# Kernel tuning notes

Hardware: AMD Instinct MI355X
Metric: run time of the kernel (lower is better)

The kernel has to match this reference:

```python
import jax, jax.numpy as jnp
import numpy as np

BN_EPS = 1e-5

def setup_inputs() -> dict:
    key = jax.random.key(0)
    k1, k2, k3 = jax.random.split(key, 3)
    N, T, C = 20000, 35, 4
    cin, cout = 7, 128
    h = cout // 2  # 64
    voxels = jax.random.normal(k1, (N, T, C), dtype=jnp.float32)
    # Linear params (torch default init scale ~ 1/sqrt(cin))
    W = jax.random.normal(k2, (h, cin), dtype=jnp.float32) / np.sqrt(cin)
    b = jax.random.normal(k3, (h,), dtype=jnp.float32) * 0.01
    gamma = jnp.ones((h,), dtype=jnp.float32)
    beta = jnp.zeros((h,), dtype=jnp.float32)
    return {"voxels": voxels, "W": W, "b": b, "gamma": gamma, "beta": beta}

def reference(voxels, W, b, gamma, beta):
    N, T, C = voxels.shape
    # mask of non-empty points: rows whose channel-sum is nonzero
    mask = (voxels.sum(axis=-1, keepdims=True) != 0)              # [N,T,1]
    counts = mask.sum(axis=1, keepdims=True).astype(voxels.dtype)  # [N,1,1]
    voxels_mean = voxels.sum(axis=1, keepdims=True) / counts       # [N,1,C]
    rel = voxels[:, :, :3] - voxels_mean[:, :, :3]                 # [N,T,3]
    aug = jnp.concatenate([voxels, rel], axis=-1)                  # [N,T,C+3]
    x = aug.reshape(-1, aug.shape[-1])                             # [N*T, 7]
    # Linear
    x = x @ W.T + b                                                # [N*T, h]
    # BatchNorm1d (training mode: batch stats, biased variance)
    mu = x.mean(axis=0)
    var = jnp.mean(jnp.square(x - mu), axis=0)
    x = (x - mu) / jnp.sqrt(var + BN_EPS) * gamma + beta
    # ReLU
    x = jnp.maximum(x, 0.0)
    x = x.reshape(N, T, -1)                                        # [N,T,h]
    agg = x.max(axis=1, keepdims=True)                             # [N,1,h]
    out = jnp.concatenate([x, jnp.broadcast_to(agg, x.shape)], axis=-1)  # [N,T,2h]
    return out
```

## Files before the change

kernel.cpp:

```cpp
#include <hip/hip_runtime.h>


#define NVOX   20000
#define TDIM   35
#define NCH    128
#define HID    64
#define NTF    700000.0f
#define EPS    1e-5f
#define NBLK_A 256
#define SCALE_OFF (NBLK_A * 35)
#define SHIFT_OFF (NBLK_A * 35 + 64)

__global__ __launch_bounds__(256) void vfe_stats(const float* __restrict__ vox,
                                                 float* __restrict__ ws) {
  const int lane = threadIdx.x & 63;
  const int wid  = threadIdx.x >> 6;
  const int gwave  = (blockIdx.x * 256 + threadIdx.x) >> 6;
  const int nwaves = NBLK_A * 4;

  float m2[28], sv[7];
#pragma unroll
  for (int i = 0; i < 28; ++i) m2[i] = 0.f;
#pragma unroll
  for (int i = 0; i < 7; ++i) sv[i] = 0.f;

  for (int n = gwave; n < NVOX; n += nwaves) {
    float4 row = make_float4(0.f, 0.f, 0.f, 0.f);
    if (lane < TDIM) row = *(const float4*)(vox + (size_t)n * (TDIM * 4) + lane * 4);
    float rowsum = (row.x + row.y) + (row.z + row.w);
    float cnt = (float)__popcll(__ballot((lane < TDIM) && (rowsum != 0.f)));
    float s0 = row.x, s1 = row.y, s2 = row.z;
#pragma unroll
    for (int off = 32; off; off >>= 1) {
      s0 += __shfl_down(s0, off);
      s1 += __shfl_down(s1, off);
      s2 += __shfl_down(s2, off);
    }
    float mx = __shfl(s0, 0) / cnt;
    float my = __shfl(s1, 0) / cnt;
    float mz = __shfl(s2, 0) / cnt;
    if (lane < TDIM) {
      float a[7] = {row.x, row.y, row.z, row.w, row.x - mx, row.y - my, row.z - mz};
      int idx = 0;
#pragma unroll
      for (int j = 0; j < 7; ++j) {
        sv[j] += a[j];
#pragma unroll
        for (int k = j; k < 7; ++k) { m2[idx] = fmaf(a[j], a[k], m2[idx]); ++idx; }
      }
    }
  }

  __shared__ float part[4][35];
#pragma unroll
  for (int i = 0; i < 35; ++i) {
    float v = (i < 28) ? m2[i] : sv[i - 28];
#pragma unroll
    for (int off = 32; off; off >>= 1) v += __shfl_down(v, off);
    if (lane == 0) part[wid][i] = v;
  }
  __syncthreads();
  if (threadIdx.x < 35)
    ws[blockIdx.x * 35 + threadIdx.x] =
        part[0][threadIdx.x] + part[1][threadIdx.x] +
        part[2][threadIdx.x] + part[3][threadIdx.x];
}

__global__ void vfe_bnparams(const float* __restrict__ W, const float* __restrict__ b,
                             const float* __restrict__ gamma, const float* __restrict__ beta,
                             float* __restrict__ ws) {
  __shared__ float stats[35];
  for (int i = threadIdx.x; i < 35; i += 64) {
    float acc = 0.f;
    for (int p = 0; p < NBLK_A; ++p) acc += ws[p * 35 + i];
    stats[i] = acc;
  }
  __syncthreads();

  const int c = threadIdx.x;
  float m2[7][7];
  {
    int idx = 0;
    for (int j = 0; j < 7; ++j)
      for (int k = j; k < 7; ++k) { float v = stats[idx++]; m2[j][k] = v; m2[k][j] = v; }
  }
  float w[7];
#pragma unroll
  for (int j = 0; j < 7; ++j) w[j] = W[c * 7 + j];
  float bc = b[c];

  float wdots = 0.f;
#pragma unroll
  for (int j = 0; j < 7; ++j) wdots = fmaf(w[j], stats[28 + j], wdots);
  float q = 0.f;
#pragma unroll
  for (int j = 0; j < 7; ++j) {
    float t = 0.f;
#pragma unroll
    for (int k = 0; k < 7; ++k) t = fmaf(w[k], m2[j][k], t);
    q = fmaf(w[j], t, q);
  }
  float sx  = wdots + NTF * bc;
  float sxx = q + 2.f * bc * wdots + NTF * bc * bc;
  float mu  = sx / NTF;
  float var = sxx / NTF - mu * mu;
  float scale = gamma[c] / sqrtf(var + EPS);
  float shift = beta[c] + scale * (bc - mu);
  ws[SCALE_OFF + c] = scale;
  ws[SHIFT_OFF + c] = shift;
}

__global__ __launch_bounds__(256) void vfe_encode(const float* __restrict__ vox,
                                                  const float* __restrict__ W,
                                                  const float* __restrict__ ws,
                                                  float* __restrict__ out) {
  const int lane = threadIdx.x & 63;
  const int n = (blockIdx.x * 256 + threadIdx.x) >> 6;
  if (n >= NVOX) return;

  float4 row = make_float4(0.f, 0.f, 0.f, 0.f);
  if (lane < TDIM) row = *(const float4*)(vox + (size_t)n * (TDIM * 4) + lane * 4);
  float rowsum = (row.x + row.y) + (row.z + row.w);
  float cnt = (float)__popcll(__ballot((lane < TDIM) && (rowsum != 0.f)));
  float s0 = row.x, s1 = row.y, s2 = row.z;
#pragma unroll
  for (int off = 32; off; off >>= 1) {
    s0 += __shfl_down(s0, off);
    s1 += __shfl_down(s1, off);
    s2 += __shfl_down(s2, off);
  }
  const float r4 = row.x - __shfl(s0, 0) / cnt;
  const float r5 = row.y - __shfl(s1, 0) / cnt;
  const float r6 = row.z - __shfl(s2, 0) / cnt;

  const float w0 = W[lane * 7 + 0], w1 = W[lane * 7 + 1], w2 = W[lane * 7 + 2],
              w3 = W[lane * 7 + 3], w4 = W[lane * 7 + 4], w5 = W[lane * 7 + 5],
              w6 = W[lane * 7 + 6];
  const float scale = ws[SCALE_OFF + lane];
  const float shift = ws[SHIFT_OFF + lane];

  float* op = out + (size_t)n * (TDIM * NCH) + lane;
  float agg = 0.f;
#pragma unroll
  for (int t = 0; t < TDIM; ++t) {
    float d = w0 * __shfl(row.x, t);
    d = fmaf(w1, __shfl(row.y, t), d);
    d = fmaf(w2, __shfl(row.z, t), d);
    d = fmaf(w3, __shfl(row.w, t), d);
    d = fmaf(w4, __shfl(r4, t), d);
    d = fmaf(w5, __shfl(r5, t), d);
    d = fmaf(w6, __shfl(r6, t), d);
    float y = fmaf(d, scale, shift);
    y = fmaxf(y, 0.f);
    agg = fmaxf(agg, y);
    op[t * NCH] = y;
  }
#pragma unroll
  for (int t = 0; t < TDIM; ++t) op[t * NCH + HID] = agg;
}

extern "C" void kernel_launch(void* const* d_in, const int* in_sizes, int n_in,
                              void* d_out, int out_size, void* d_ws, size_t ws_size,
                              hipStream_t stream) {
  const float* vox   = (const float*)d_in[0];
  const float* W     = (const float*)d_in[1];
  const float* b     = (const float*)d_in[2];
  const float* gamma = (const float*)d_in[3];
  const float* beta  = (const float*)d_in[4];
  float* out = (float*)d_out;
  float* ws  = (float*)d_ws;

  vfe_stats<<<NBLK_A, 256, 0, stream>>>(vox, ws);
  vfe_bnparams<<<1, 64, 0, stream>>>(W, b, gamma, beta, ws);
  vfe_encode<<<(NVOX * 64) / 256, 256, 0, stream>>>(vox, W, ws, out);
}
```

Baseline: 397.8 us.

## Fold BN scale into weights and vectorize encode stores via LDS-staged rows

The BN parameter kernel now folds scale into the linear weights and merges the relative-coordinate terms algebraically, so the encoder needs four FMAs per output plus a per-voxel base. The encode kernel stages each voxel's rows in shared memory and remaps lanes so each thread handles four channels across a quarter of the time steps. Output is written with float4 stores, which should give wider, coalesced writes on this output-bandwidth-bound kernel. It adds a block barrier and a cross-lane max reduction, and it relies on NVOX being divisible by 4 now that the bounds check is removed.

```diff
diff --git a/kernel.cpp b/kernel.cpp
--- a/kernel.cpp
+++ b/kernel.cpp
@@ -8,8 +8,7 @@
 #define NTF    700000.0f
 #define EPS    1e-5f
 #define NBLK_A 256
-#define SCALE_OFF (NBLK_A * 35)
-#define SHIFT_OFF (NBLK_A * 35 + 64)
+#define PARAM_OFF (NBLK_A * 35)
 
 __global__ __launch_bounds__(256) void vfe_stats(const float* __restrict__ vox,
                                                  float* __restrict__ ws) {
@@ -36,9 +35,10 @@
       s1 += __shfl_down(s1, off);
       s2 += __shfl_down(s2, off);
     }
-    float mx = __shfl(s0, 0) / cnt;
-    float my = __shfl(s1, 0) / cnt;
-    float mz = __shfl(s2, 0) / cnt;
+    float rc = 1.f / cnt;
+    float mx = __shfl(s0, 0) * rc;
+    float my = __shfl(s1, 0) * rc;
+    float mz = __shfl(s2, 0) * rc;
     if (lane < TDIM) {
       float a[7] = {row.x, row.y, row.z, row.w, row.x - mx, row.y - my, row.z - mz};
       int idx = 0;
@@ -106,17 +106,26 @@
   float var = sxx / NTF - mu * mu;
   float scale = gamma[c] / sqrtf(var + EPS);
   float shift = beta[c] + scale * (bc - mu);
-  ws[SCALE_OFF + c] = scale;
-  ws[SHIFT_OFF + c] = shift;
+
+  float* p = ws + PARAM_OFF + c * 8;
+  p[0] = scale * (w[0] + w[4]);
+  p[1] = scale * (w[1] + w[5]);
+  p[2] = scale * (w[2] + w[6]);
+  p[3] = scale * w[3];
+  p[4] = scale * w[4];
+  p[5] = scale * w[5];
+  p[6] = scale * w[6];
+  p[7] = shift;
 }
 
 __global__ __launch_bounds__(256) void vfe_encode(const float* __restrict__ vox,
-                                                  const float* __restrict__ W,
                                                   const float* __restrict__ ws,
                                                   float* __restrict__ out) {
   const int lane = threadIdx.x & 63;
+  const int wid  = threadIdx.x >> 6;
   const int n = (blockIdx.x * 256 + threadIdx.x) >> 6;
-  if (n >= NVOX) return;
+
+  __shared__ float4 rows[4][64];
 
   float4 row = make_float4(0.f, 0.f, 0.f, 0.f);
   if (lane < TDIM) row = *(const float4*)(vox + (size_t)n * (TDIM * 4) + lane * 4);
@@ -129,34 +138,60 @@
     s1 += __shfl_down(s1, off);
     s2 += __shfl_down(s2, off);
   }
-  const float r4 = row.x - __shfl(s0, 0) / cnt;
-  const float r5 = row.y - __shfl(s1, 0) / cnt;
-  const float r6 = row.z - __shfl(s2, 0) / cnt;
-
-  const float w0 = W[lane * 7 + 0], w1 = W[lane * 7 + 1], w2 = W[lane * 7 + 2],
-              w3 = W[lane * 7 + 3], w4 = W[lane * 7 + 4], w5 = W[lane * 7 + 5],
-              w6 = W[lane * 7 + 6];
-  const float scale = ws[SCALE_OFF + lane];
-  const float shift = ws[SHIFT_OFF + lane];
-
-  float* op = out + (size_t)n * (TDIM * NCH) + lane;
-  float agg = 0.f;
-#pragma unroll
-  for (int t = 0; t < TDIM; ++t) {
-    float d = w0 * __shfl(row.x, t);
-    d = fmaf(w1, __shfl(row.y, t), d);
-    d = fmaf(w2, __shfl(row.z, t), d);
-    d = fmaf(w3, __shfl(row.w, t), d);
-    d = fmaf(w4, __shfl(r4, t), d);
-    d = fmaf(w5, __shfl(r5, t), d);
-    d = fmaf(w6, __shfl(r6, t), d);
-    float y = fmaf(d, scale, shift);
-    y = fmaxf(y, 0.f);
-    agg = fmaxf(agg, y);
-    op[t * NCH] = y;
-  }
-#pragma unroll
-  for (int t = 0; t < TDIM; ++t) op[t * NCH + HID] = agg;
+  float rc = 1.f / cnt;
+  const float mx = __shfl(s0, 0) * rc;
+  const float my = __shfl(s1, 0) * rc;
+  const float mz = __shfl(s2, 0) * rc;
+
+  rows[wid][lane] = row;
+  __syncthreads();
+
+  const int tg = lane >> 4;
+  const int c4 = (lane & 15) << 2;
+
+  const float4* pars = (const float4*)(ws + PARAM_OFF);
+  float4 wv[4], wr[4];
+  float base[4], agg[4];
+#pragma unroll
+  for (int i = 0; i < 4; ++i) {
+    wv[i] = pars[(c4 + i) * 2];
+    wr[i] = pars[(c4 + i) * 2 + 1];
+    base[i] = wr[i].w - (wr[i].x * mx + wr[i].y * my + wr[i].z * mz);
+    agg[i] = 0.f;
+  }
+
+  float* op = out + (size_t)n * (TDIM * NCH);
+#pragma unroll
+  for (int k = 0; k < 9; ++k) {
+    const int t = 4 * k + tg;
+    if (t < TDIM) {
+      float4 v = rows[wid][t];
+      float y[4];
+#pragma unroll
+      for (int i = 0; i < 4; ++i) {
+        float d = fmaf(wv[i].x, v.x, base[i]);
+        d = fmaf(wv[i].y, v.y, d);
+        d = fmaf(wv[i].z, v.z, d);
+        d = fmaf(wv[i].w, v.w, d);
+        d = fmaxf(d, 0.f);
+        agg[i] = fmaxf(agg[i], d);
+        y[i] = d;
+      }
+      *(float4*)(op + t * NCH + c4) = make_float4(y[0], y[1], y[2], y[3]);
+    }
+  }
+
+#pragma unroll
+  for (int i = 0; i < 4; ++i) {
+    agg[i] = fmaxf(agg[i], __shfl_xor(agg[i], 16));
+    agg[i] = fmaxf(agg[i], __shfl_xor(agg[i], 32));
+  }
+  const float4 av = make_float4(agg[0], agg[1], agg[2], agg[3]);
+#pragma unroll
+  for (int k = 0; k < 9; ++k) {
+    const int t = 4 * k + tg;
+    if (t < TDIM) *(float4*)(op + t * NCH + HID + c4) = av;
+  }
 }
 
 extern "C" void kernel_launch(void* const* d_in, const int* in_sizes, int n_in,
@@ -172,5 +207,5 @@
 
   vfe_stats<<<NBLK_A, 256, 0, stream>>>(vox, ws);
   vfe_bnparams<<<1, 64, 0, stream>>>(W, b, gamma, beta, ws);
-  vfe_encode<<<(NVOX * 64) / 256, 256, 0, stream>>>(vox, W, ws, out);
-}
+  vfe_encode<<<NVOX / 4, 256, 0, stream>>>(vox, ws, out);
+}
```

New measurement: 407.7 us. 1.02x slower.
